# Kernel optimization log

Hardware: AMD Instinct MI355X
Metric: run time of the kernel (lower is better)

Reference implementation:

```python
import jax, jax.numpy as jnp
import numpy as np

NUM_USERS = 100000
NUM_ITEMS = 200000
EMBED_DIM = 128
NUM_EDGES = 2000000
N_LAYERS = 2
EPS = 1e-5


def layer_norm(x, gamma, beta):
    m = jnp.mean(x, axis=-1, keepdims=True)
    v = jnp.mean(jnp.square(x - m), axis=-1, keepdims=True)
    return gamma * (x - m) * jax.lax.rsqrt(v + EPS) + beta


def setup_inputs() -> dict:
    key = jax.random.key(0)
    k1, k2, k3, k4, k5 = jax.random.split(key, 5)
    user_emb = jax.random.normal(k1, (NUM_USERS, EMBED_DIM), dtype=jnp.float32) * 0.1
    item_emb = jax.random.normal(k2, (NUM_ITEMS, EMBED_DIM), dtype=jnp.float32) * 0.1
    # COO edge list for the user-item bipartite graph; iu_adj = ui_adj^T
    rows = jax.random.randint(k3, (NUM_EDGES,), 0, NUM_USERS, dtype=jnp.int32)
    cols = jax.random.randint(k4, (NUM_EDGES,), 0, NUM_ITEMS, dtype=jnp.int32)
    # positive normalized edge weights (e.g. sym-normalized adjacency values)
    vals = jax.random.uniform(k5, (NUM_EDGES,), dtype=jnp.float32) * (1.0 / 16.0)
    ln_gamma = jnp.ones((EMBED_DIM,), dtype=jnp.float32)
    ln_beta = jnp.zeros((EMBED_DIM,), dtype=jnp.float32)
    return {"user_emb": user_emb, "item_emb": item_emb, "vals": vals,
            "ln_gamma": ln_gamma, "ln_beta": ln_beta, "rows": rows, "cols": cols}


def reference(user_emb, item_emb, vals, ln_gamma, ln_beta, rows, cols):
    # SpMM via gather + segment_sum (COO). dropout is identity (eval / p=0).
    u_emb, i_emb = user_emb, item_emb
    for _ in range(N_LAYERS):
        # u_temp = ui_adj @ i_emb : [NUM_USERS, D]
        u_temp = jax.ops.segment_sum(vals[:, None] * i_emb[cols], rows,
                                     num_segments=NUM_USERS)
        # i_temp = iu_adj @ u_emb : [NUM_ITEMS, D]  (iu_adj = ui_adj^T)
        i_temp = jax.ops.segment_sum(vals[:, None] * u_emb[rows], cols,
                                     num_segments=NUM_ITEMS)
        u_emb = layer_norm(u_emb + u_temp, ln_gamma, ln_beta)
        i_emb = layer_norm(i_emb + i_temp, ln_gamma, ln_beta)
    return u_emb, i_emb
```

## Files before the change

### kernel.cpp

```cpp
#include <hip/hip_runtime.h>

#define EPS 1e-5f
typedef long long ll;
typedef unsigned int uint;

#define CHUNK   16384
#define NCPAD   256
#define NBMAX   2048

__device__ __forceinline__ uint bf_round(float x) {
    uint u = __float_as_uint(x);
    return (u + 0x7FFFu + ((u >> 16) & 1u)) >> 16;
}
__device__ __forceinline__ uint pack2(float a, float b) {
    return bf_round(a) | (bf_round(b) << 16);
}
__device__ __forceinline__ float unpack_lo(uint u) { return __uint_as_float(u << 16); }
__device__ __forceinline__ float unpack_hi(uint u) { return __uint_as_float(u & 0xFFFF0000u); }

__global__ __launch_bounds__(256) void hist_conv_k(
    const int* __restrict__ rows, const int* __restrict__ cols,
    int* __restrict__ counts, int ne, int nu, int NB, int hb,
    const float* __restrict__ ue, const float* __restrict__ ie,
    uint4* __restrict__ bfout, int nuT, int totT)
{
    int b = blockIdx.x;
    if (b < hb) {
        __shared__ int hist[NBMAX];
        for (int i = threadIdx.x; i < NB; i += 256) hist[i] = 0;
        __syncthreads();
        ll base0 = (ll)b * CHUNK;
        ll items = 2LL * ne;
        int n2 = (int)min((ll)CHUNK, items - base0);
        for (int k = threadIdx.x; k < n2; k += 256) {
            ll e = base0 + k;
            int bucket = (e < ne) ? rows[e] : nu + cols[e - ne];
            atomicAdd(&hist[bucket >> 8], 1);
        }
        __syncthreads();
        for (int i = threadIdx.x; i < NB; i += 256)
            counts[(ll)i * NCPAD + b] = hist[i];
    } else {
        int t = (b - hb) * 256 + threadIdx.x;
        if (t < totT) {
            const float4* src = (t < nuT) ? (const float4*)(ue + (ll)t * 8)
                                          : (const float4*)(ie + (ll)(t - nuT) * 8);
            float4 f0 = src[0], f1 = src[1];
            uint4 q;
            q.x = pack2(f0.x, f0.y); q.y = pack2(f0.z, f0.w);
            q.z = pack2(f1.x, f1.y); q.w = pack2(f1.z, f1.w);
            bfout[t] = q;
        }
    }
}

__global__ __launch_bounds__(256) void s1_kernel(
    const int* __restrict__ counts, int* __restrict__ base,
    int* __restrict__ binT, int nchunk)
{
    int b = blockIdx.x;
    int t = threadIdx.x;
    int v = (t < nchunk) ? counts[(ll)b * NCPAD + t] : 0;
    __shared__ int sm[256];
    sm[t] = v; __syncthreads();
    for (int off = 1; off < 256; off <<= 1) {
        int a = (t >= off) ? sm[t - off] : 0;
        __syncthreads();
        sm[t] += a;
        __syncthreads();
    }
    base[(ll)b * NCPAD + t] = sm[t] - v;
    if (t == 255) binT[b] = sm[255];
}

__global__ __launch_bounds__(256) void s2_kernel(
    const int* __restrict__ binT, int* __restrict__ binptr,
    int* __restrict__ rowptr, int NB, int Nrow, int total)
{
    __shared__ int sm[256];
    int t = threadIdx.x;
    const int PER = NBMAX / 256;
    int loc[PER]; int s = 0;
#pragma unroll
    for (int k = 0; k < PER; k++) {
        int i = t * PER + k;
        loc[k] = (i < NB) ? binT[i] : 0;
        s += loc[k];
    }
    sm[t] = s; __syncthreads();
    for (int off = 1; off < 256; off <<= 1) {
        int a = (t >= off) ? sm[t - off] : 0;
        __syncthreads();
        sm[t] += a;
        __syncthreads();
    }
    int run = sm[t] - s;
#pragma unroll
    for (int k = 0; k < PER; k++) {
        int i = t * PER + k;
        if (i < NB) binptr[i] = run;
        run += loc[k];
    }
    if (t == 0) { binptr[NB] = total; rowptr[Nrow] = total; }
}

__global__ __launch_bounds__(256) void p2_kernel(
    const int* __restrict__ rows, const int* __restrict__ cols,
    const float* __restrict__ vals,
    const int* __restrict__ base, const int* __restrict__ binptr,
    int4* __restrict__ tmp, int ne, int nu, int NB)
{
    __shared__ int cur[NBMAX];
    int c = blockIdx.x;
    for (int i = threadIdx.x; i < NB; i += 256)
        cur[i] = binptr[i] + base[(ll)i * NCPAD + c];
    __syncthreads();
    ll base0 = (ll)c * CHUNK;
    ll items = 2LL * ne;
    int n2 = (int)min((ll)CHUNK, items - base0);
    for (int k = threadIdx.x; k < n2; k += 256) {
        ll e = base0 + k;
        int bucket, src; float v;
        if (e < ne) { bucket = rows[e]; src = cols[e]; v = vals[e]; }
        else        { ll e2 = e - ne; bucket = nu + cols[e2]; src = rows[e2]; v = vals[e2]; }
        int slot = atomicAdd(&cur[bucket >> 8], 1);
        tmp[slot] = make_int4(bucket, src, __float_as_int(v), 0);
    }
}

__global__ __launch_bounds__(256) void p3_kernel(
    const int4* __restrict__ tmp, const int* __restrict__ binptr,
    int* __restrict__ rowptr, int2* __restrict__ csr)
{
    __shared__ int hist[256];
    __shared__ int sm[256];
    __shared__ int fineExcl[256];
    int b = blockIdx.x;
    int t = threadIdx.x;
    int s0 = binptr[b], s1 = binptr[b + 1];
    hist[t] = 0; __syncthreads();
    for (int i = s0 + t; i < s1; i += 256) {
        int4 it = tmp[i];
        atomicAdd(&hist[it.x & 255], 1);
    }
    __syncthreads();
    int v = hist[t];
    sm[t] = v; __syncthreads();
    for (int off = 1; off < 256; off <<= 1) {
        int a = (t >= off) ? sm[t - off] : 0;
        __syncthreads();
        sm[t] += a;
        __syncthreads();
    }
    fineExcl[t] = sm[t] - v;
    __syncthreads();
    rowptr[(b << 8) + t] = s0 + fineExcl[t];
    hist[t] = fineExcl[t];
    __syncthreads();
    for (int i = s0 + t; i < s1; i += 256) {
        int4 it = tmp[i];
        int r = atomicAdd(&hist[it.x & 255], 1);
        csr[s0 + r] = make_int2(it.y, it.z);
    }
}

template<bool OUT_BF>
__global__ __launch_bounds__(256) void gather_ln_k(
    const uint4* __restrict__ srcU,
    const uint4* __restrict__ srcI,
    const uint4* __restrict__ resU, const uint4* __restrict__ resI,
    void* __restrict__ outU, void* __restrict__ outI,
    const int* __restrict__ rowptr, const int2* __restrict__ csr,
    const float* __restrict__ gamma, const float* __restrict__ beta,
    int nu, int N)
{
    int w = blockIdx.x * 4 + (threadIdx.x >> 6);
    if (w >= N) return;
    int lane = threadIdx.x & 63;
    int sub  = lane >> 4;
    int l16  = lane & 15;

    const uint4* tbl;
    const uint4* res;
    void* out;
    if (w < nu) {
        tbl = srcU;
        res = resU + (ll)w * 16;
        out = OUT_BF ? (void*)((uint4*)outU + (ll)w * 16)
                     : (void*)((float4*)outU + (ll)w * 32);
    } else {
        int k = w - nu;
        tbl = srcI;
        res = resI + (ll)k * 16;
        out = OUT_BF ? (void*)((uint4*)outI + (ll)k * 16)
                     : (void*)((float4*)outI + (ll)k * 32);
    }

    int start = rowptr[w];
    int end   = rowptr[w + 1];

    float a0=0.f,a1=0.f,a2=0.f,a3=0.f,a4=0.f,a5=0.f,a6=0.f,a7=0.f;

    if (start < end) {
        int i0 = start + sub;
        int2 ec = csr[i0 < end ? i0 : end - 1];
        for (int j = start; j < end; j += 4) {
            int2 en;
            int jn = j + 4;
            if (jn < end) {
                int i1 = jn + sub;
                en = csr[i1 < end ? i1 : end - 1];
            }
            float v = ((j + sub) < end) ? __int_as_float(ec.y) : 0.0f;
            uint4 q = tbl[(((uint)ec.x) << 4) + l16];
            a0 += v * unpack_lo(q.x); a1 += v * unpack_hi(q.x);
            a2 += v * unpack_lo(q.y); a3 += v * unpack_hi(q.y);
            a4 += v * unpack_lo(q.z); a5 += v * unpack_hi(q.z);
            a6 += v * unpack_lo(q.w); a7 += v * unpack_hi(q.w);
            ec = en;
        }
    }

#define MRG(x) x += __shfl_xor(x, 16, 64); x += __shfl_xor(x, 32, 64)
    MRG(a0); MRG(a1); MRG(a2); MRG(a3); MRG(a4); MRG(a5); MRG(a6); MRG(a7);
#undef MRG

    uint4 r = res[l16];
    a0 += unpack_lo(r.x); a1 += unpack_hi(r.x);
    a2 += unpack_lo(r.y); a3 += unpack_hi(r.y);
    a4 += unpack_lo(r.z); a5 += unpack_hi(r.z);
    a6 += unpack_lo(r.w); a7 += unpack_hi(r.w);

    float s  = a0+a1+a2+a3+a4+a5+a6+a7;
    float ss = a0*a0+a1*a1+a2*a2+a3*a3+a4*a4+a5*a5+a6*a6+a7*a7;
#pragma unroll
    for (int off = 8; off > 0; off >>= 1) {
        s  += __shfl_xor(s, off, 64);
        ss += __shfl_xor(ss, off, 64);
    }
    float m   = s * (1.0f / 128.0f);
    float var = ss * (1.0f / 128.0f) - m * m;
    float inv = rsqrtf(var + EPS);

    float4 g0 = ((const float4*)gamma)[l16 * 2];
    float4 g1 = ((const float4*)gamma)[l16 * 2 + 1];
    float4 b0 = ((const float4*)beta)[l16 * 2];
    float4 b1 = ((const float4*)beta)[l16 * 2 + 1];
    float o0 = g0.x * (a0 - m) * inv + b0.x;
    float o1 = g0.y * (a1 - m) * inv + b0.y;
    float o2 = g0.z * (a2 - m) * inv + b0.z;
    float o3 = g0.w * (a3 - m) * inv + b0.w;
    float o4 = g1.x * (a4 - m) * inv + b1.x;
    float o5 = g1.y * (a5 - m) * inv + b1.y;
    float o6 = g1.z * (a6 - m) * inv + b1.z;
    float o7 = g1.w * (a7 - m) * inv + b1.w;

    if (sub == 0) {
        if (OUT_BF) {
            uint4 q;
            q.x = pack2(o0, o1); q.y = pack2(o2, o3);
            q.z = pack2(o4, o5); q.w = pack2(o6, o7);
            ((uint4*)out)[l16] = q;
        } else {
            ((float4*)out)[l16 * 2]     = make_float4(o0, o1, o2, o3);
            ((float4*)out)[l16 * 2 + 1] = make_float4(o4, o5, o6, o7);
        }
    }
}

extern "C" void kernel_launch(void* const* d_in, const int* in_sizes, int n_in,
                              void* d_out, int out_size, void* d_ws, size_t ws_size,
                              hipStream_t stream)
{
    const float* user_emb = (const float*)d_in[0];
    const float* item_emb = (const float*)d_in[1];
    const float* vals     = (const float*)d_in[2];
    const float* gamma    = (const float*)d_in[3];
    const float* beta     = (const float*)d_in[4];
    const int*   rows     = (const int*)d_in[5];
    const int*   cols     = (const int*)d_in[6];

    const int nu = in_sizes[0] / 128;
    const int ni = in_sizes[1] / 128;
    const int ne = in_sizes[2];
    const int N  = nu + ni;
    const int total = 2 * ne;

    float* dout   = (float*)d_out;
    float* dout_u = dout;
    float* dout_i = dout + (ll)nu * 128;

    uint* bf_u = (uint*)d_out;
    uint* bf_i = bf_u + (ll)nu * 64;

    const int NB = (N + 255) >> 8;
    const int hb = (total + CHUNK - 1) / CHUNK;

    int*  rowptr  = (int*)d_ws;
    int*  counts  = rowptr + (ll)NB * 256;
    int*  base    = counts + (ll)NB * 256;
    int*  binT    = base + (ll)NB * 256;
    int*  binptr  = binT + NBMAX;
    int2* csr     = (int2*)(binptr + NBMAX);
    uint* wu_out  = (uint*)(csr + total);
    uint* wi_out  = wu_out + (ll)nu * 64;
    int4* tmp     = (int4*)wu_out;

    const int totT = (nu + ni) * 16;
    const int tb   = (totT + 255) / 256;

    hist_conv_k<<<hb + tb, 256, 0, stream>>>(rows, cols, counts, ne, nu, NB, hb,
                                             user_emb, item_emb,
                                             (uint4*)bf_u, nu * 16, totT);
    s1_kernel<<<NB, 256, 0, stream>>>(counts, base, binT, hb);
    s2_kernel<<<1, 256, 0, stream>>>(binT, binptr, rowptr, NB, N, total);
    p2_kernel<<<hb, 256, 0, stream>>>(rows, cols, vals, base, binptr, tmp, ne, nu, NB);
    p3_kernel<<<NB, 256, 0, stream>>>(tmp, binptr, rowptr, csr);

    const int gblocks = (N + 3) / 4;

    gather_ln_k<true><<<gblocks, 256, 0, stream>>>(
        (const uint4*)bf_i, (const uint4*)bf_u,
        (const uint4*)bf_u, (const uint4*)bf_i,
        wu_out, wi_out,
        rowptr, csr, gamma, beta, nu, N);

    gather_ln_k<false><<<gblocks, 256, 0, stream>>>(
        (const uint4*)wi_out, (const uint4*)wu_out,
        (const uint4*)wu_out, (const uint4*)wi_out,
        dout_u, dout_i,
        rowptr, csr, gamma, beta, nu, N);
}
```

Baseline: 798.7 us.

## Pack CSR-build temp records, stage bins in LDS, and pipeline gather loads

Temp records in the CSR build shrink from int4 to int2 by packing the fine bucket index into the top 8 bits of the source id. This halves the scatter and reread traffic. The p3 pass stages each bin in shared memory so the second pass does not reread global memory. CHUNK is halved with NCPAD doubled, and s1 scans two counts per thread, which gives more p2 blocks. The gather loop is software-pipelined one row ahead using packed float2 FMAs. The 24-bit source id limit is enough for these sizes, but the 64KB LDS stage may reduce p3 occupancy.

```diff
diff --git a/kernel.cpp b/kernel.cpp
--- a/kernel.cpp
+++ b/kernel.cpp
@@ -3,10 +3,12 @@
 #define EPS 1e-5f
 typedef long long ll;
 typedef unsigned int uint;
-
-#define CHUNK   16384
-#define NCPAD   256
+typedef float f32x2 __attribute__((ext_vector_type(2)));
+
+#define CHUNK   8192
+#define NCPAD   512
 #define NBMAX   2048
+#define P3CAP   8192
 
 __device__ __forceinline__ uint bf_round(float x) {
     uint u = __float_as_uint(x);
@@ -60,16 +62,21 @@
 {
     int b = blockIdx.x;
     int t = threadIdx.x;
-    int v = (t < nchunk) ? counts[(ll)b * NCPAD + t] : 0;
+    int i0 = 2 * t, i1 = 2 * t + 1;
+    int v0 = (i0 < nchunk) ? counts[(ll)b * NCPAD + i0] : 0;
+    int v1 = (i1 < nchunk) ? counts[(ll)b * NCPAD + i1] : 0;
+    int s = v0 + v1;
     __shared__ int sm[256];
-    sm[t] = v; __syncthreads();
+    sm[t] = s; __syncthreads();
     for (int off = 1; off < 256; off <<= 1) {
         int a = (t >= off) ? sm[t - off] : 0;
         __syncthreads();
         sm[t] += a;
         __syncthreads();
     }
-    base[(ll)b * NCPAD + t] = sm[t] - v;
+    int excl = sm[t] - s;
+    base[(ll)b * NCPAD + i0] = excl;
+    base[(ll)b * NCPAD + i1] = excl + v0;
     if (t == 255) binT[b] = sm[255];
 }
 
@@ -108,7 +115,7 @@
     const int* __restrict__ rows, const int* __restrict__ cols,
     const float* __restrict__ vals,
     const int* __restrict__ base, const int* __restrict__ binptr,
-    int4* __restrict__ tmp, int ne, int nu, int NB)
+    int2* __restrict__ tmp, int ne, int nu, int NB)
 {
     __shared__ int cur[NBMAX];
     int c = blockIdx.x;
@@ -124,24 +131,32 @@
         if (e < ne) { bucket = rows[e]; src = cols[e]; v = vals[e]; }
         else        { ll e2 = e - ne; bucket = nu + cols[e2]; src = rows[e2]; v = vals[e2]; }
         int slot = atomicAdd(&cur[bucket >> 8], 1);
-        tmp[slot] = make_int4(bucket, src, __float_as_int(v), 0);
+        tmp[slot] = make_int2(((bucket & 255) << 24) | src, __float_as_int(v));
     }
 }
 
 __global__ __launch_bounds__(256) void p3_kernel(
-    const int4* __restrict__ tmp, const int* __restrict__ binptr,
+    const int2* __restrict__ tmp, const int* __restrict__ binptr,
     int* __restrict__ rowptr, int2* __restrict__ csr)
 {
     __shared__ int hist[256];
     __shared__ int sm[256];
-    __shared__ int fineExcl[256];
+    __shared__ int2 stage[P3CAP];
     int b = blockIdx.x;
     int t = threadIdx.x;
     int s0 = binptr[b], s1 = binptr[b + 1];
+    int n = s1 - s0;
+    bool inLds = (n <= P3CAP);
     hist[t] = 0; __syncthreads();
-    for (int i = s0 + t; i < s1; i += 256) {
-        int4 it = tmp[i];
-        atomicAdd(&hist[it.x & 255], 1);
+    if (inLds) {
+        for (int i = t; i < n; i += 256) {
+            int2 it = tmp[s0 + i];
+            stage[i] = it;
+            atomicAdd(&hist[(uint)it.x >> 24], 1);
+        }
+    } else {
+        for (int i = t; i < n; i += 256)
+            atomicAdd(&hist[(uint)tmp[s0 + i].x >> 24], 1);
     }
     __syncthreads();
     int v = hist[t];
@@ -152,22 +167,29 @@
         sm[t] += a;
         __syncthreads();
     }
-    fineExcl[t] = sm[t] - v;
+    int excl = sm[t] - v;
     __syncthreads();
-    rowptr[(b << 8) + t] = s0 + fineExcl[t];
-    hist[t] = fineExcl[t];
+    rowptr[(b << 8) + t] = s0 + excl;
+    hist[t] = excl;
     __syncthreads();
-    for (int i = s0 + t; i < s1; i += 256) {
-        int4 it = tmp[i];
-        int r = atomicAdd(&hist[it.x & 255], 1);
-        csr[s0 + r] = make_int2(it.y, it.z);
+    if (inLds) {
+        for (int i = t; i < n; i += 256) {
+            int2 it = stage[i];
+            int r = atomicAdd(&hist[(uint)it.x >> 24], 1);
+            csr[s0 + r] = make_int2(it.x & 0xFFFFFF, it.y);
+        }
+    } else {
+        for (int i = t; i < n; i += 256) {
+            int2 it = tmp[s0 + i];
+            int r = atomicAdd(&hist[(uint)it.x >> 24], 1);
+            csr[s0 + r] = make_int2(it.x & 0xFFFFFF, it.y);
+        }
     }
 }
 
 template<bool OUT_BF>
 __global__ __launch_bounds__(256) void gather_ln_k(
-    const uint4* __restrict__ srcU,
-    const uint4* __restrict__ srcI,
+    const uint4* __restrict__ srcU, const uint4* __restrict__ srcI,
     const uint4* __restrict__ resU, const uint4* __restrict__ resI,
     void* __restrict__ outU, void* __restrict__ outI,
     const int* __restrict__ rowptr, const int2* __restrict__ csr,
@@ -199,27 +221,49 @@
     int start = rowptr[w];
     int end   = rowptr[w + 1];
 
-    float a0=0.f,a1=0.f,a2=0.f,a3=0.f,a4=0.f,a5=0.f,a6=0.f,a7=0.f;
+    f32x2 a01 = {0.f, 0.f}, a23 = {0.f, 0.f}, a45 = {0.f, 0.f}, a67 = {0.f, 0.f};
+
+#define FMA8(q, vv) {                                                   \
+        f32x2 b;                                                        \
+        b[0] = unpack_lo(q.x); b[1] = unpack_hi(q.x); a01 = vv * b + a01; \
+        b[0] = unpack_lo(q.y); b[1] = unpack_hi(q.y); a23 = vv * b + a23; \
+        b[0] = unpack_lo(q.z); b[1] = unpack_hi(q.z); a45 = vv * b + a45; \
+        b[0] = unpack_lo(q.w); b[1] = unpack_hi(q.w); a67 = vv * b + a67; }
 
     if (start < end) {
         int i0 = start + sub;
-        int2 ec = csr[i0 < end ? i0 : end - 1];
-        for (int j = start; j < end; j += 4) {
-            int2 en;
-            int jn = j + 4;
-            if (jn < end) {
-                int i1 = jn + sub;
-                en = csr[i1 < end ? i1 : end - 1];
+        int2 ecC = csr[i0 < end ? i0 : end - 1];
+        int2 ecN = ecC;
+        if (start + 4 < end) {
+            int i1 = start + 4 + sub;
+            ecN = csr[i1 < end ? i1 : end - 1];
+        }
+        uint4 qC = tbl[(((uint)ecC.x) << 4) + l16];
+
+        int j = start;
+        for (; j + 4 < end; j += 4) {
+            int jnn = j + 8;
+            int2 ecF = ecN;
+            if (jnn < end) {
+                int i2 = jnn + sub;
+                ecF = csr[i2 < end ? i2 : end - 1];
             }
-            float v = ((j + sub) < end) ? __int_as_float(ec.y) : 0.0f;
-            uint4 q = tbl[(((uint)ec.x) << 4) + l16];
-            a0 += v * unpack_lo(q.x); a1 += v * unpack_hi(q.x);
-            a2 += v * unpack_lo(q.y); a3 += v * unpack_hi(q.y);
-            a4 += v * unpack_lo(q.z); a5 += v * unpack_hi(q.z);
-            a6 += v * unpack_lo(q.w); a7 += v * unpack_hi(q.w);
-            ec = en;
-        }
-    }
+            uint4 qN = tbl[(((uint)ecN.x) << 4) + l16];
+            float v = __int_as_float(ecC.y);
+            f32x2 vv = {v, v};
+            FMA8(qC, vv);
+            ecC = ecN; ecN = ecF; qC = qN;
+        }
+        {
+            float v = ((j + sub) < end) ? __int_as_float(ecC.y) : 0.0f;
+            f32x2 vv = {v, v};
+            FMA8(qC, vv);
+        }
+    }
+#undef FMA8
+
+    float a0 = a01[0], a1 = a01[1], a2 = a23[0], a3 = a23[1];
+    float a4 = a45[0], a5 = a45[1], a6 = a67[0], a7 = a67[1];
 
 #define MRG(x) x += __shfl_xor(x, 16, 64); x += __shfl_xor(x, 32, 64)
     MRG(a0); MRG(a1); MRG(a2); MRG(a3); MRG(a4); MRG(a5); MRG(a6); MRG(a7);
@@ -298,13 +342,13 @@
 
     int*  rowptr  = (int*)d_ws;
     int*  counts  = rowptr + (ll)NB * 256;
-    int*  base    = counts + (ll)NB * 256;
-    int*  binT    = base + (ll)NB * 256;
+    int*  base    = counts + (ll)NB * NCPAD;
+    int*  binT    = base + (ll)NB * NCPAD;
     int*  binptr  = binT + NBMAX;
     int2* csr     = (int2*)(binptr + NBMAX);
     uint* wu_out  = (uint*)(csr + total);
     uint* wi_out  = wu_out + (ll)nu * 64;
-    int4* tmp     = (int4*)wu_out;
+    int2* tmp     = (int2*)wu_out;
 
     const int totT = (nu + ni) * 16;
     const int tb   = (totT + 255) / 256;
```

Result: faster. 741.9 us (-7.1%).
